# Optimization experiments

Measured on AMD Instinct MI355X. Metric: run time of the kernel, lower is better.

Reference implementation:

```python
import jax, jax.numpy as jnp
import numpy as np


def setup_inputs() -> dict:
    key = jax.random.key(0)
    k_x, k_w, k_s, k_b = jax.random.split(key, 4)
    B, S, D_IN, D_OUT = 8, 2048, 4096, 4096
    x = jax.random.normal(k_x, (B, S, D_IN), dtype=jnp.float32)
    # int8-valued weights stored as int32 (values in [-128, 127])
    quantized_weights = jax.random.randint(k_w, (D_OUT, D_IN), -128, 128, dtype=jnp.int32)
    scales = jax.random.normal(k_s, (D_OUT,), dtype=jnp.float32)
    bias = jax.random.normal(k_b, (D_OUT,), dtype=jnp.float32)
    return {"x": x, "quantized_weights": quantized_weights, "scales": scales, "bias": bias}


def reference(x, quantized_weights, scales, bias):
    # Per-output-channel dequant: W[o, i] = q[o, i] * scales[o]
    dequantized_weight = quantized_weights.astype(x.dtype) * scales[:, None].astype(x.dtype)
    # F.linear: y = x @ W^T + b
    return jnp.einsum('bsi,oi->bso', x, dequantized_weight) + bias.astype(x.dtype)
```

## Files before the change

kernel.cpp:

```cpp
#include <hip/hip_runtime.h>

#define M_DIM 16384
#define N_DIM 4096
#define K_DIM 4096
#define NT 32

typedef __attribute__((ext_vector_type(4))) float f32x4;
typedef __attribute__((ext_vector_type(8))) short bf16x8;
typedef __attribute__((ext_vector_type(4))) int   i32x4;

__device__ __forceinline__ short f2bf(float f) {
    unsigned int u = __builtin_bit_cast(unsigned int, f);
    u += 0x7FFFu + ((u >> 16) & 1u);
    return (short)(u >> 16);
}

__global__ __launch_bounds__(256)
void quant_kernel(const float* __restrict__ x, const int* __restrict__ q,
                  char* __restrict__ x8, char* __restrict__ w8,
                  float* __restrict__ rs) {
    const int tid = threadIdx.x;
    if (blockIdx.x < M_DIM) {
        const int row = blockIdx.x;
        const float* xr = x + (size_t)row * K_DIM;
        f32x4 v[4];
        float am = 0.f;
#pragma unroll
        for (int p = 0; p < 4; ++p) {
            v[p] = *(const f32x4*)(xr + p * 1024 + tid * 4);
#pragma unroll
            for (int e = 0; e < 4; ++e) am = fmaxf(am, fabsf(v[p][e]));
        }
#pragma unroll
        for (int off = 32; off >= 1; off >>= 1)
            am = fmaxf(am, __shfl_xor(am, off, 64));
        __shared__ float smax[4];
        if ((tid & 63) == 0) smax[tid >> 6] = am;
        __syncthreads();
        am = fmaxf(fmaxf(smax[0], smax[1]), fmaxf(smax[2], smax[3]));
        const float inv = am > 0.f ? 127.f / am : 0.f;
        if (tid == 0) rs[row] = am / 127.f;
        int* o32 = (int*)(x8 + (size_t)row * K_DIM);
#pragma unroll
        for (int p = 0; p < 4; ++p) {
            const int b0 = (int)rintf(v[p][0] * inv);
            const int b1 = (int)rintf(v[p][1] * inv);
            const int b2 = (int)rintf(v[p][2] * inv);
            const int b3 = (int)rintf(v[p][3] * inv);
            o32[p * 256 + tid] = (b0 & 255) | ((b1 & 255) << 8) | ((b2 & 255) << 16) | ((b3 & 255) << 24);
        }
    } else {
        const long n = (long)N_DIM * K_DIM;
        long i = ((long)(blockIdx.x - M_DIM) * 256 + tid) * 16;
        const long stride = 2048L * 256 * 16;
        for (; i < n; i += stride) {
            i32x4 o;
#pragma unroll
            for (int j = 0; j < 4; ++j) {
                i32x4 a = *(const i32x4*)(q + i + j * 4);
                o[j] = (a[0] & 255) | ((a[1] & 255) << 8) | ((a[2] & 255) << 16) | ((a[3] & 255) << 24);
            }
            *(i32x4*)(w8 + i) = o;
        }
    }
}

__device__ __forceinline__ void load_lds16(const void* g, void* l) {
    __builtin_amdgcn_global_load_lds((const __attribute__((address_space(1))) void*)g,
                                     (__attribute__((address_space(3))) void*)l, 16, 0, 0);
}

#define BAR() __builtin_amdgcn_s_barrier()
#define VM(n) asm volatile("s_waitcnt vmcnt(" #n ")" ::: "memory")

__global__ __launch_bounds__(512, 2)
void gemm8p_i8(const char* __restrict__ A, const char* __restrict__ Bw,
               const float* __restrict__ rs, const float* __restrict__ scales,
               const float* __restrict__ bias, float* __restrict__ out) {
    __shared__ char lds[2][4][128 * 128];

    const int tid  = threadIdx.x;
    const int lane = tid & 63;
    const int w    = tid >> 6;
    const int wm   = w >> 2;
    const int wn   = w & 3;
    const int lrow = lane & 15;
    const int lkg  = lane >> 4;
    const int sx   = lane & 7;

    const int nwg = gridDim.x;
    const int swz = (blockIdx.x & 7) * (nwg >> 3) + (blockIdx.x >> 3);
    const int bn  = (swz & 15) * 256;
    const int bm  = (swz >> 4) * 256;

    const char* aS[2];
    const char* bS[2];
#pragma unroll
    for (int L = 0; L < 2; ++L) {
        const int c   = L * 512 + tid;
        const int row = c >> 3;
        const int kc  = (c & 7) ^ (row & 7);
        const int mA  = bm + ((row >> 6) << 7) + (row & 63);
        const int nB  = bn + ((row >> 5) << 6) + (row & 31);
        aS[L] = A  + (size_t)mA * K_DIM + kc * 16;
        bS[L] = Bw + (size_t)nB * K_DIM + kc * 16;
    }
    const int wofs = w << 10;

#define STAGE_A(buf, q, kt) do { \
    char* d = &lds[buf][q][wofs]; \
    const long ko = (long)(kt) * 128 + (long)(q) * (64 * (long)K_DIM); \
    load_lds16(aS[0] + ko, d); \
    load_lds16(aS[1] + ko, d + 8192); \
} while (0)

#define STAGE_B(buf, nh, kt) do { \
    char* d = &lds[buf][2 + (nh)][wofs]; \
    const long ko = (long)(kt) * 128 + (long)(nh) * (32 * (long)K_DIM); \
    load_lds16(bS[0] + ko, d); \
    load_lds16(bS[1] + ko, d + 8192); \
} while (0)

    const int aoff = (wm << 6) + lrow;
    const int boff = (wn << 5) + lrow;

#define RD_A(buf, q, sub, ks) \
    (*(const i32x4*)&lds[buf][q][((aoff + (sub) * 16) << 7) + (((((ks) << 2) + lkg) ^ sx) << 4)])
#define RD_B(buf, nh, sub, ks) \
    (*(const i32x4*)&lds[buf][2 + (nh)][((boff + (sub) * 16) << 7) + (((((ks) << 2) + lkg) ^ sx) << 4)])

    i32x4 acc[8][4];
#pragma unroll
    for (int i = 0; i < 8; ++i)
#pragma unroll
        for (int j = 0; j < 4; ++j)
            acc[i][j] = (i32x4){0, 0, 0, 0};

    i32x4 aF[4][2], bF0[2][2], bF1[2][2];

#define LOAD_AF(buf, q) do { \
    _Pragma("unroll") for (int ii = 0; ii < 4; ++ii) { \
        aF[ii][0] = RD_A(buf, q, ii, 0); aF[ii][1] = RD_A(buf, q, ii, 1); } \
} while (0)
#define LOAD_BF(dst, buf, nh) do { \
    _Pragma("unroll") for (int jj = 0; jj < 2; ++jj) { \
        dst[jj][0] = RD_B(buf, nh, jj, 0); dst[jj][1] = RD_B(buf, nh, jj, 1); } \
} while (0)
#define MMA_Q(mh, nh, BREG) do { \
    __builtin_amdgcn_s_setprio(1); \
    _Pragma("unroll") for (int ii = 0; ii < 4; ++ii) \
    _Pragma("unroll") for (int jj = 0; jj < 2; ++jj) \
    _Pragma("unroll") for (int ks = 0; ks < 2; ++ks) \
        acc[(mh) * 4 + ii][(nh) * 2 + jj] = __builtin_amdgcn_mfma_i32_16x16x64_i8( \
            aF[ii][ks], BREG[jj][ks], acc[(mh) * 4 + ii][(nh) * 2 + jj], 0, 0, 0); \
    __builtin_amdgcn_s_setprio(0); \
} while (0)

    STAGE_A(0, 0, 0); STAGE_A(0, 1, 0); STAGE_B(0, 0, 0); STAGE_B(0, 1, 0);
    STAGE_A(1, 0, 1); STAGE_B(1, 0, 1); STAGE_B(1, 1, 1);
    VM(6);
    BAR();

    for (int it = 0; it < NT / 2; ++it) {
        const int kt  = it * 2;
        const bool s2 = (kt + 2 < NT);
        const bool s3 = (kt + 3 < NT);

        LOAD_AF(0, 0); LOAD_BF(bF0, 0, 0);
        STAGE_A(1, 1, kt + 1);
        BAR(); MMA_Q(0, 0, bF0); BAR();
        LOAD_BF(bF1, 0, 1);
        if (s2) STAGE_A(0, 0, kt + 2);
        BAR(); MMA_Q(0, 1, bF1); BAR();
        LOAD_AF(0, 1);
        if (s2) STAGE_B(0, 0, kt + 2);
        BAR(); MMA_Q(1, 0, bF0); BAR();
        if (s2) { STAGE_B(0, 1, kt + 2); VM(6); } else { VM(0); }
        BAR(); MMA_Q(1, 1, bF1); BAR();
        LOAD_AF(1, 0); LOAD_BF(bF0, 1, 0);
        if (s2) STAGE_A(0, 1, kt + 2);
        BAR(); MMA_Q(0, 0, bF0); BAR();
        LOAD_BF(bF1, 1, 1);
        if (s3) STAGE_A(1, 0, kt + 3);
        BAR(); MMA_Q(0, 1, bF1); BAR();
        LOAD_AF(1, 1);
        if (s3) STAGE_B(1, 0, kt + 3);
        BAR(); MMA_Q(1, 0, bF0); BAR();
        if (s3) { STAGE_B(1, 1, kt + 3); VM(6); }
        BAR(); MMA_Q(1, 1, bF1); BAR();
    }

#pragma unroll
    for (int i = 0; i < 8; ++i) {
        const int r0 = bm + (wm << 7) + i * 16 + (lkg << 2);
        const f32x4 rsv = *(const f32x4*)&rs[r0];
#pragma unroll
        for (int j = 0; j < 4; ++j) {
            const int col = bn + (wn << 6) + j * 16 + lrow;
            const float sc = scales[col];
            const float bb = bias[col];
#pragma unroll
            for (int r = 0; r < 4; ++r)
                out[(size_t)(r0 + r) * N_DIM + col] = (float)acc[i][j][r] * (rsv[r] * sc) + bb;
        }
    }
#undef STAGE_A
#undef STAGE_B
#undef RD_A
#undef RD_B
#undef LOAD_AF
#undef LOAD_BF
#undef MMA_Q
}

__global__ __launch_bounds__(256)
void gemm_fallback(const float* __restrict__ Xf, const int* __restrict__ Qw,
                   const float* __restrict__ scales, const float* __restrict__ bias,
                   float* __restrict__ out) {
    __shared__ short a_lds[128 * 64];
    __shared__ short b_lds[128 * 64];
    const int tid  = threadIdx.x;
    const int lane = tid & 63;
    const int wid  = tid >> 6;
    const int wm   = wid >> 1;
    const int wn   = wid & 1;
    const int bn = (blockIdx.x % (N_DIM / 128)) * 128;
    const int bm = (blockIdx.x / (N_DIM / 128)) * 128;
    const int lrow = lane & 15;
    const int lkg  = lane >> 4;

    f32x4 acc[4][4];
#pragma unroll
    for (int i = 0; i < 4; ++i)
#pragma unroll
        for (int j = 0; j < 4; ++j)
            acc[i][j] = (f32x4){0.f, 0.f, 0.f, 0.f};

    for (int k0 = 0; k0 < K_DIM; k0 += 64) {
#pragma unroll
        for (int t = 0; t < 4; ++t) {
            const int ch  = t * 256 + tid;
            const int row = ch >> 3;
            const int kc  = (ch & 7) ^ (row & 7);
            {
                const float* sa = Xf + (size_t)(bm + row) * K_DIM + k0 + kc * 8;
                f32x4 a0 = *(const f32x4*)sa;
                f32x4 a1 = *(const f32x4*)(sa + 4);
                bf16x8 r;
                r[0] = f2bf(a0[0]); r[1] = f2bf(a0[1]); r[2] = f2bf(a0[2]); r[3] = f2bf(a0[3]);
                r[4] = f2bf(a1[0]); r[5] = f2bf(a1[1]); r[6] = f2bf(a1[2]); r[7] = f2bf(a1[3]);
                *(bf16x8*)&a_lds[ch * 8] = r;
            }
            {
                const int* sb = Qw + (size_t)(bn + row) * K_DIM + k0 + kc * 8;
                i32x4 q0 = *(const i32x4*)sb;
                i32x4 q1 = *(const i32x4*)(sb + 4);
                bf16x8 r;
                r[0] = f2bf((float)q0[0]); r[1] = f2bf((float)q0[1]);
                r[2] = f2bf((float)q0[2]); r[3] = f2bf((float)q0[3]);
                r[4] = f2bf((float)q1[0]); r[5] = f2bf((float)q1[1]);
                r[6] = f2bf((float)q1[2]); r[7] = f2bf((float)q1[3]);
                *(bf16x8*)&b_lds[ch * 8] = r;
            }
        }
        __syncthreads();
#pragma unroll
        for (int ks = 0; ks < 2; ++ks) {
            const int kgl = ks * 4 + lkg;
            bf16x8 af[4], bfr[4];
#pragma unroll
            for (int i = 0; i < 4; ++i) {
                const int am = wm * 64 + i * 16 + lrow;
                af[i]  = *(const bf16x8*)&a_lds[am * 64 + ((kgl ^ (am & 7)) << 3)];
                const int bnn = wn * 64 + i * 16 + lrow;
                bfr[i] = *(const bf16x8*)&b_lds[bnn * 64 + ((kgl ^ (bnn & 7)) << 3)];
            }
#pragma unroll
            for (int i = 0; i < 4; ++i)
#pragma unroll
                for (int j = 0; j < 4; ++j)
                    acc[i][j] = __builtin_amdgcn_mfma_f32_16x16x32_bf16(af[i], bfr[j], acc[i][j], 0, 0, 0);
        }
        __syncthreads();
    }
#pragma unroll
    for (int j = 0; j < 4; ++j) {
        const int col = bn + wn * 64 + j * 16 + lrow;
        const float s  = scales[col];
        const float bb = bias[col];
#pragma unroll
        for (int i = 0; i < 4; ++i) {
            const int row0 = bm + wm * 64 + i * 16 + lkg * 4;
#pragma unroll
            for (int r = 0; r < 4; ++r)
                out[(size_t)(row0 + r) * N_DIM + col] = acc[i][j][r] * s + bb;
        }
    }
}

extern "C" void kernel_launch(void* const* d_in, const int* in_sizes, int n_in,
                              void* d_out, int out_size, void* d_ws, size_t ws_size,
                              hipStream_t stream) {
    const float* x      = (const float*)d_in[0];
    const int*   qw     = (const int*)d_in[1];
    const float* scales = (const float*)d_in[2];
    const float* bias   = (const float*)d_in[3];
    float* out = (float*)d_out;

    const size_t x_elems = (size_t)M_DIM * K_DIM;
    const size_t w_elems = (size_t)N_DIM * K_DIM;
    const size_t need    = x_elems + w_elems + M_DIM * sizeof(float);

    if (ws_size >= need) {
        char*  x8 = (char*)d_ws;
        char*  w8 = x8 + x_elems;
        float* rs = (float*)(w8 + w_elems);
        quant_kernel<<<M_DIM + 2048, 256, 0, stream>>>(x, qw, x8, w8, rs);
        const dim3 grid((M_DIM / 256) * (N_DIM / 256));
        gemm8p_i8<<<grid, 512, 0, stream>>>(x8, w8, rs, scales, bias, out);
    } else {
        const dim3 grid((M_DIM / 128) * (N_DIM / 128));
        gemm_fallback<<<grid, 256, 0, stream>>>(x, qw, scales, bias, out);
    }
}
```

Measured before the change: 343.3 us.

## Make int8 GEMM persistent over four M tiles with continuous K-pipeline

The int8 GEMM now launches a fixed grid of 256 workgroups. Each one walks four 256-row M tiles in sequence for its N tile, and the double-buffered LDS prefetch runs across tile boundaries so the pipeline never drains between tiles. Each stage now issues its MFMAs in two half-stages with fewer barriers, and setprio wraps the whole LDS-read-plus-MFMA region. This is meant to remove per-tile prologue and epilogue costs and reduce barrier overhead. In exchange, the fp32 epilogue stores sit inline in the main loop and stall the pipeline, and wave-level occupancy balancing depends on 256 workgroups fitting the CU count.

```diff
diff --git a/kernel.cpp b/kernel.cpp
--- a/kernel.cpp
+++ b/kernel.cpp
@@ -3,7 +3,7 @@
 #define M_DIM 16384
 #define N_DIM 4096
 #define K_DIM 4096
-#define NT 32
+#define NTOT 128
 
 typedef __attribute__((ext_vector_type(4))) float f32x4;
 typedef __attribute__((ext_vector_type(8))) short bf16x8;
@@ -72,11 +72,13 @@
 
 #define BAR() __builtin_amdgcn_s_barrier()
 #define VM(n) asm volatile("s_waitcnt vmcnt(" #n ")" ::: "memory")
+#define SETP1 __builtin_amdgcn_s_setprio(1)
+#define SETP0 __builtin_amdgcn_s_setprio(0)
 
 __global__ __launch_bounds__(512, 2)
-void gemm8p_i8(const char* __restrict__ A, const char* __restrict__ Bw,
-               const float* __restrict__ rs, const float* __restrict__ scales,
-               const float* __restrict__ bias, float* __restrict__ out) {
+void gemm_persist(const char* __restrict__ A, const char* __restrict__ Bw,
+                  const float* __restrict__ rs, const float* __restrict__ scales,
+                  const float* __restrict__ bias, float* __restrict__ out) {
     __shared__ char lds[2][4][128 * 128];
 
     const int tid  = threadIdx.x;
@@ -88,10 +90,9 @@
     const int lkg  = lane >> 4;
     const int sx   = lane & 7;
 
-    const int nwg = gridDim.x;
-    const int swz = (blockIdx.x & 7) * (nwg >> 3) + (blockIdx.x >> 3);
+    const int swz = ((int)blockIdx.x & 7) * 32 + ((int)blockIdx.x >> 3);
     const int bn  = (swz & 15) * 256;
-    const int bm  = (swz >> 4) * 256;
+    const int bm0 = (swz >> 4) * 256;
 
     const char* aS[2];
     const char* bS[2];
@@ -100,23 +101,26 @@
         const int c   = L * 512 + tid;
         const int row = c >> 3;
         const int kc  = (c & 7) ^ (row & 7);
-        const int mA  = bm + ((row >> 6) << 7) + (row & 63);
-        const int nB  = bn + ((row >> 5) << 6) + (row & 31);
+        const int mA  = bm0 + ((row >> 6) << 7) + (row & 63);
+        const int nB  = bn  + ((row >> 5) << 6) + (row & 31);
         aS[L] = A  + (size_t)mA * K_DIM + kc * 16;
         bS[L] = Bw + (size_t)nB * K_DIM + kc * 16;
     }
     const int wofs = w << 10;
 
-#define STAGE_A(buf, q, kt) do { \
+#define KO_A(g, q) ((long)((g) >> 5) * (4096L * K_DIM) + (long)((g) & 31) * 128 + (long)(q) * (64L * K_DIM))
+#define KO_B(g, nh) ((long)((g) & 31) * 128 + (long)(nh) * (32L * K_DIM))
+
+#define STAGE_A(buf, q, g) do { \
     char* d = &lds[buf][q][wofs]; \
-    const long ko = (long)(kt) * 128 + (long)(q) * (64 * (long)K_DIM); \
+    const long ko = KO_A(g, q); \
     load_lds16(aS[0] + ko, d); \
     load_lds16(aS[1] + ko, d + 8192); \
 } while (0)
 
-#define STAGE_B(buf, nh, kt) do { \
+#define STAGE_B(buf, nh, g) do { \
     char* d = &lds[buf][2 + (nh)][wofs]; \
-    const long ko = (long)(kt) * 128 + (long)(nh) * (32 * (long)K_DIM); \
+    const long ko = KO_B(g, nh); \
     load_lds16(bS[0] + ko, d); \
     load_lds16(bS[1] + ko, d + 8192); \
 } while (0)
@@ -147,63 +151,64 @@
         dst[jj][0] = RD_B(buf, nh, jj, 0); dst[jj][1] = RD_B(buf, nh, jj, 1); } \
 } while (0)
 #define MMA_Q(mh, nh, BREG) do { \
-    __builtin_amdgcn_s_setprio(1); \
     _Pragma("unroll") for (int ii = 0; ii < 4; ++ii) \
     _Pragma("unroll") for (int jj = 0; jj < 2; ++jj) \
     _Pragma("unroll") for (int ks = 0; ks < 2; ++ks) \
         acc[(mh) * 4 + ii][(nh) * 2 + jj] = __builtin_amdgcn_mfma_i32_16x16x64_i8( \
             aF[ii][ks], BREG[jj][ks], acc[(mh) * 4 + ii][(nh) * 2 + jj], 0, 0, 0); \
-    __builtin_amdgcn_s_setprio(0); \
-} while (0)
-
-    STAGE_A(0, 0, 0); STAGE_A(0, 1, 0); STAGE_B(0, 0, 0); STAGE_B(0, 1, 0);
+} while (0)
+
+    STAGE_A(0, 0, 0); STAGE_B(0, 0, 0); STAGE_B(0, 1, 0); STAGE_A(0, 1, 0);
     STAGE_A(1, 0, 1); STAGE_B(1, 0, 1); STAGE_B(1, 1, 1);
-    VM(6);
-    BAR();
-
-    for (int it = 0; it < NT / 2; ++it) {
-        const int kt  = it * 2;
-        const bool s2 = (kt + 2 < NT);
-        const bool s3 = (kt + 3 < NT);
-
-        LOAD_AF(0, 0); LOAD_BF(bF0, 0, 0);
-        STAGE_A(1, 1, kt + 1);
-        BAR(); MMA_Q(0, 0, bF0); BAR();
-        LOAD_BF(bF1, 0, 1);
-        if (s2) STAGE_A(0, 0, kt + 2);
-        BAR(); MMA_Q(0, 1, bF1); BAR();
-        LOAD_AF(0, 1);
-        if (s2) STAGE_B(0, 0, kt + 2);
-        BAR(); MMA_Q(1, 0, bF0); BAR();
-        if (s2) { STAGE_B(0, 1, kt + 2); VM(6); } else { VM(0); }
-        BAR(); MMA_Q(1, 1, bF1); BAR();
-        LOAD_AF(1, 0); LOAD_BF(bF0, 1, 0);
-        if (s2) STAGE_A(0, 1, kt + 2);
-        BAR(); MMA_Q(0, 0, bF0); BAR();
-        LOAD_BF(bF1, 1, 1);
-        if (s3) STAGE_A(1, 0, kt + 3);
-        BAR(); MMA_Q(0, 1, bF1); BAR();
-        LOAD_AF(1, 1);
-        if (s3) STAGE_B(1, 0, kt + 3);
-        BAR(); MMA_Q(1, 0, bF0); BAR();
-        if (s3) { STAGE_B(1, 1, kt + 3); VM(6); }
-        BAR(); MMA_Q(1, 1, bF1); BAR();
-    }
-
-#pragma unroll
-    for (int i = 0; i < 8; ++i) {
-        const int r0 = bm + (wm << 7) + i * 16 + (lkg << 2);
-        const f32x4 rsv = *(const f32x4*)&rs[r0];
-#pragma unroll
-        for (int j = 0; j < 4; ++j) {
-            const int col = bn + (wn << 6) + j * 16 + lrow;
-            const float sc = scales[col];
-            const float bb = bias[col];
-#pragma unroll
-            for (int r = 0; r < 4; ++r)
-                out[(size_t)(r0 + r) * N_DIM + col] = (float)acc[i][j][r] * (rsv[r] * sc) + bb;
-        }
-    }
+
+    for (int g = 0; g < NTOT; ++g) {
+        const int buf = g & 1;
+
+        if (g + 1 < NTOT) STAGE_A(buf ^ 1, 1, g + 1);
+        if (g == NTOT - 1) { VM(2); } else { VM(10); }
+        BAR();
+        SETP1;
+        LOAD_AF(buf, 0);
+        LOAD_BF(bF0, buf, 0);
+        MMA_Q(0, 0, bF0);
+        LOAD_BF(bF1, buf, 1);
+        MMA_Q(0, 1, bF1);
+        SETP0;
+        BAR();
+
+        if (g + 2 < NTOT) {
+            STAGE_A(buf, 0, g + 2); STAGE_B(buf, 0, g + 2); STAGE_B(buf, 1, g + 2);
+        }
+        if (g == NTOT - 1) { VM(0); } else if (g == NTOT - 2) { VM(8); } else { VM(14); }
+        BAR();
+        SETP1;
+        LOAD_AF(buf, 1);
+        MMA_Q(1, 0, bF0);
+        MMA_Q(1, 1, bF1);
+        SETP0;
+        BAR();
+
+        if ((g & 31) == 31) {
+            const int bm = bm0 + (g >> 5) * 4096;
+#pragma unroll
+            for (int i = 0; i < 8; ++i) {
+                const int r0 = bm + (wm << 7) + i * 16 + (lkg << 2);
+                const f32x4 rsv = *(const f32x4*)&rs[r0];
+#pragma unroll
+                for (int j = 0; j < 4; ++j) {
+                    const int col = bn + (wn << 6) + j * 16 + lrow;
+                    const float sc = scales[col];
+                    const float bb = bias[col];
+#pragma unroll
+                    for (int r = 0; r < 4; ++r)
+                        out[(size_t)(r0 + r) * N_DIM + col] = (float)acc[i][j][r] * (rsv[r] * sc) + bb;
+                    acc[i][j] = (i32x4){0, 0, 0, 0};
+                }
+            }
+        }
+    }
+#undef KO_A
+#undef KO_B
 #undef STAGE_A
 #undef STAGE_B
 #undef RD_A
@@ -316,8 +321,7 @@
         char*  w8 = x8 + x_elems;
         float* rs = (float*)(w8 + w_elems);
         quant_kernel<<<M_DIM + 2048, 256, 0, stream>>>(x, qw, x8, w8, rs);
-        const dim3 grid((M_DIM / 256) * (N_DIM / 256));
-        gemm8p_i8<<<grid, 512, 0, stream>>>(x8, w8, rs, scales, bias, out);
+        gemm_persist<<<256, 512, 0, stream>>>(x8, w8, rs, scales, bias, out);
     } else {
         const dim3 grid((M_DIM / 128) * (N_DIM / 128));
         gemm_fallback<<<grid, 256, 0, stream>>>(x, qw, scales, bias, out);
```

Result: slower. 361.2 us (+5.2%).
